# Optimization experiments

Hardware: AMD Instinct MI355X
Metric: run time of the kernel (lower is better)

Reference implementation:

```python
import jax, jax.numpy as jnp
import numpy as np

NUM_THRESHOLDS = 200
N = 4_000_000
KEPS = 1e-07
EPS = 1e-06


def _make_thresholds(num_thresholds=NUM_THRESHOLDS):
    inner = [(i + 1) * 1.0 / (num_thresholds - 1) for i in range(num_thresholds - 2)]
    return jnp.asarray([0.0 - KEPS] + inner + [1.0 + KEPS], dtype=jnp.float32)


def setup_inputs() -> dict:
    key = jax.random.key(0)
    k1, k2 = jax.random.split(key)
    predictions = jax.random.uniform(k1, (N,), dtype=jnp.float32)  # in [0,1]
    labels = jax.random.randint(k2, (N,), 0, 2, dtype=jnp.int32)
    thresholds = _make_thresholds()
    return {"predictions": predictions, "labels": labels, "thresholds": thresholds}


def reference(predictions, labels, thresholds):
    # Confusion matrix at all thresholds: [T, N] broadcast compare, reduce over N.
    lab_pos = labels.astype(bool)  # [N]
    pred_pos = predictions[None, :] > thresholds[:, None]  # [T, N] bool
    lab_pos_b = jnp.broadcast_to(lab_pos[None, :], pred_pos.shape)
    tp = jnp.sum(jnp.logical_and(lab_pos_b, pred_pos), axis=1).astype(jnp.float32)
    fn = jnp.sum(jnp.logical_and(lab_pos_b, ~pred_pos), axis=1).astype(jnp.float32)
    fp = jnp.sum(jnp.logical_and(~lab_pos_b, pred_pos), axis=1).astype(jnp.float32)
    tn = jnp.sum(jnp.logical_and(~lab_pos_b, ~pred_pos), axis=1).astype(jnp.float32)
    # Trapezoidal AUC over (FPR, TPR)
    rec = (tp + EPS) / (tp + fn + EPS)          # y (TPR)
    fp_rate = fp / (fp + tn + EPS)              # x (FPR)
    x, y = fp_rate, rec
    auc = jnp.sum((x[:-1] - x[1:]) * (y[:-1] + y[1:]) * 0.5)
    return auc
```

## Files before the change

kernel.cpp:

```cpp
#include <hip/hip_runtime.h>

#define NTH    200
#define NBINS  201
#define NBLKH  1024
#define HTPB   256
#define HWAVES 4


__device__ __forceinline__ void bin4(const float4 p, const int4 l,
                                     const float* __restrict__ s_th,
                                     unsigned int* __restrict__ my) {
    float pv[4] = {p.x, p.y, p.z, p.w};
    int   lv[4] = {l.x, l.y, l.z, l.w};
#pragma unroll
    for (int j = 0; j < 4; ++j) {
        float pp = pv[j];
        int k0 = (int)(pp * 199.0f);
        k0 = k0 > 198 ? 198 : k0;
        float ta = s_th[k0];
        float tb = s_th[k0 + 1];
        int g = k0 + ((ta < pp) ? ((tb < pp) ? 2 : 1) : 0);
        unsigned int add = 1u | ((unsigned int)(lv[j] != 0) << 16);
        atomicAdd(&my[g], add);
    }
}

__global__ void __launch_bounds__(HTPB)
auroc_hist_kernel(const float* __restrict__ preds,
                  const int*   __restrict__ labels,
                  const float* __restrict__ thresholds,
                  unsigned int* __restrict__ part,
                  unsigned int* __restrict__ ticket,
                  int n) {
    __shared__ float        s_th[NTH];
    __shared__ unsigned int s_hist[HWAVES][NBINS];

    const int t    = threadIdx.x;
    const int wave = t >> 6;

    if (blockIdx.x == 0 && t == 0) *ticket = 0u;

    for (int i = t; i < HWAVES * NBINS; i += HTPB)
        ((unsigned int*)s_hist)[i] = 0u;
    for (int i = t; i < NTH; i += HTPB)
        s_th[i] = thresholds[i];
    __syncthreads();

    unsigned int* my = s_hist[wave];

    const int gid = blockIdx.x * HTPB + t;
    const int S   = gridDim.x * HTPB;
    const int n4  = n >> 2;
    const float4* p4 = (const float4*)preds;
    const int4*   l4 = (const int4*)labels;

    int i = gid;
    for (; i + 3 * S < n4; i += 4 * S) {
        float4 pa = p4[i];
        float4 pb = p4[i + S];
        float4 pc = p4[i + 2 * S];
        float4 pd = p4[i + 3 * S];
        int4   la = l4[i];
        int4   lb = l4[i + S];
        int4   lc = l4[i + 2 * S];
        int4   ld = l4[i + 3 * S];
        bin4(pa, la, s_th, my);
        bin4(pb, lb, s_th, my);
        bin4(pc, lc, s_th, my);
        bin4(pd, ld, s_th, my);
    }
    for (; i < n4; i += S) {
        bin4(p4[i], l4[i], s_th, my);
    }
    for (int k = (n4 << 2) + gid; k < n; k += S) {
        float pp = preds[k];
        int k0 = (int)(pp * 199.0f);
        k0 = k0 > 198 ? 198 : k0;
        float ta = s_th[k0];
        float tb = s_th[k0 + 1];
        int g = k0 + ((ta < pp) ? ((tb < pp) ? 2 : 1) : 0);
        unsigned int add = 1u | ((unsigned int)(labels[k] != 0) << 16);
        atomicAdd(&my[g], add);
    }
    __syncthreads();

    const int b = blockIdx.x;
    for (int i2 = t; i2 < NBINS; i2 += HTPB) {
        unsigned int v = s_hist[0][i2] + s_hist[1][i2] + s_hist[2][i2] + s_hist[3][i2];
        unsigned int pos = v >> 16;
        unsigned int neg = (v & 0xFFFFu) - pos;
        part[i2 * NBLKH + b] = (pos << 16) | neg;
    }
}

__global__ void __launch_bounds__(256)
auroc_reduce_finish(const unsigned int* __restrict__ part,
                    unsigned int* __restrict__ g_pos,
                    unsigned int* __restrict__ g_neg,
                    unsigned int* __restrict__ ticket,
                    float* __restrict__ out) {
    __shared__ unsigned int s_w[HWAVES][2];
    __shared__ unsigned int s_rank;
    __shared__ unsigned int s_pos[NBINS], s_neg[NBINS];
    __shared__ unsigned int s_sufp[NBINS + 1], s_sufn[NBINS + 1];
    __shared__ float s_x[NTH], s_y[NTH];

    const int t = threadIdx.x;
    const int r = blockIdx.x;

    uint4 v = ((const uint4*)(part + r * NBLKH))[t];
    unsigned int ap = (v.x >> 16) + (v.y >> 16) + (v.z >> 16) + (v.w >> 16);
    unsigned int an = (v.x & 0xFFFFu) + (v.y & 0xFFFFu) +
                      (v.z & 0xFFFFu) + (v.w & 0xFFFFu);
#pragma unroll
    for (int off = 32; off >= 1; off >>= 1) {
        ap += __shfl_down(ap, off, 64);
        an += __shfl_down(an, off, 64);
    }
    if ((t & 63) == 0) { s_w[t >> 6][0] = ap; s_w[t >> 6][1] = an; }
    __syncthreads();

    if (t == 0) {
        unsigned int pos = s_w[0][0] + s_w[1][0] + s_w[2][0] + s_w[3][0];
        unsigned int neg = s_w[0][1] + s_w[1][1] + s_w[2][1] + s_w[3][1];
        atomicExch(&g_pos[r], pos);
        atomicExch(&g_neg[r], neg);
        __threadfence();
        s_rank = atomicAdd(ticket, 1u);
    }
    __syncthreads();
    if (s_rank != (unsigned int)(NBINS - 1)) return;

    __threadfence();
    if (t < NBINS) {
        s_pos[t] = atomicAdd(&g_pos[t], 0u);
        s_neg[t] = atomicAdd(&g_neg[t], 0u);
    }
    if (t == 0) { s_sufp[NBINS] = 0u; s_sufn[NBINS] = 0u; }
    __syncthreads();

    if (t < NBINS) {
        unsigned int sp = 0u, sn = 0u;
        for (int k = t; k < NBINS; ++k) { sp += s_pos[k]; sn += s_neg[k]; }
        s_sufp[t] = sp;
        s_sufn[t] = sn;
    }
    __syncthreads();

    const float P   = (float)s_sufp[0];
    const float Nn  = (float)s_sufn[0];
    const float EPS = 1e-6f;

    if (t < NTH) {
        float tp = (float)s_sufp[t + 1];
        float fp = (float)s_sufn[t + 1];
        float fn = P - tp;
        float tn = Nn - fp;
        s_y[t] = (tp + EPS) / (tp + fn + EPS);
        s_x[t] = fp / (fp + tn + EPS);
    }
    __syncthreads();

    if (t == 0) {
        double auc = 0.0;
        for (int i = 0; i < NTH - 1; ++i)
            auc += (double)((s_x[i] - s_x[i + 1]) * (s_y[i] + s_y[i + 1]) * 0.5f);
        out[0] = (float)auc;
    }
}

extern "C" void kernel_launch(void* const* d_in, const int* in_sizes, int n_in,
                              void* d_out, int out_size, void* d_ws, size_t ws_size,
                              hipStream_t stream) {
    const float* preds      = (const float*)d_in[0];
    const int*   labels     = (const int*)d_in[1];
    const float* thresholds = (const float*)d_in[2];
    float*       out        = (float*)d_out;
    unsigned int* part      = (unsigned int*)d_ws;
    unsigned int* g_pos     = part + NBINS * NBLKH;
    unsigned int* g_neg     = g_pos + NBINS;
    unsigned int* ticket    = g_neg + NBINS;

    const int n = in_sizes[0];

    auroc_hist_kernel<<<NBLKH, HTPB, 0, stream>>>(preds, labels, thresholds,
                                                  part, ticket, n);
    auroc_reduce_finish<<<NBINS, 256, 0, stream>>>(part, g_pos, g_neg,
                                                   ticket, out);
}
```

Baseline: 93.79 us.

## Split reduce into separate finish kernel; unroll hist by 2; branchless bin index

Replaces the last-block ticket/atomic handoff in the reduce kernel with a third single-block finish kernel, removing atomics and threadfences. The histogram main loop now processes two float4/int4 pairs per iteration instead of four, and the bin index uses summed comparisons instead of nested selects. The label is shifted directly without a !=0 test, which assumes labels are exactly 0 or 1. Adds one extra kernel launch and reduces memory-level parallelism per thread in the hist loop.

New measurement: 87.04 us. 1.08x faster.

```diff
diff --git a/kernel.cpp b/kernel.cpp
--- a/kernel.cpp
+++ b/kernel.cpp
@@ -6,31 +6,11 @@
 #define HTPB   256
 #define HWAVES 4
 
-
-__device__ __forceinline__ void bin4(const float4 p, const int4 l,
-                                     const float* __restrict__ s_th,
-                                     unsigned int* __restrict__ my) {
-    float pv[4] = {p.x, p.y, p.z, p.w};
-    int   lv[4] = {l.x, l.y, l.z, l.w};
-#pragma unroll
-    for (int j = 0; j < 4; ++j) {
-        float pp = pv[j];
-        int k0 = (int)(pp * 199.0f);
-        k0 = k0 > 198 ? 198 : k0;
-        float ta = s_th[k0];
-        float tb = s_th[k0 + 1];
-        int g = k0 + ((ta < pp) ? ((tb < pp) ? 2 : 1) : 0);
-        unsigned int add = 1u | ((unsigned int)(lv[j] != 0) << 16);
-        atomicAdd(&my[g], add);
-    }
-}
-
 __global__ void __launch_bounds__(HTPB)
 auroc_hist_kernel(const float* __restrict__ preds,
                   const int*   __restrict__ labels,
                   const float* __restrict__ thresholds,
                   unsigned int* __restrict__ part,
-                  unsigned int* __restrict__ ticket,
                   int n) {
     __shared__ float        s_th[NTH];
     __shared__ unsigned int s_hist[HWAVES][NBINS];
@@ -38,12 +18,10 @@
     const int t    = threadIdx.x;
     const int wave = t >> 6;
 
-    if (blockIdx.x == 0 && t == 0) *ticket = 0u;
-
+    for (int i = t; i < NTH; i += HTPB)
+        s_th[i] = thresholds[i];
     for (int i = t; i < HWAVES * NBINS; i += HTPB)
         ((unsigned int*)s_hist)[i] = 0u;
-    for (int i = t; i < NTH; i += HTPB)
-        s_th[i] = thresholds[i];
     __syncthreads();
 
     unsigned int* my = s_hist[wave];
@@ -55,22 +33,42 @@
     const int4*   l4 = (const int4*)labels;
 
     int i = gid;
-    for (; i + 3 * S < n4; i += 4 * S) {
+    for (; i + S < n4; i += 2 * S) {
         float4 pa = p4[i];
+        int4   la = l4[i];
         float4 pb = p4[i + S];
-        float4 pc = p4[i + 2 * S];
-        float4 pd = p4[i + 3 * S];
-        int4   la = l4[i];
         int4   lb = l4[i + S];
-        int4   lc = l4[i + 2 * S];
-        int4   ld = l4[i + 3 * S];
-        bin4(pa, la, s_th, my);
-        bin4(pb, lb, s_th, my);
-        bin4(pc, lc, s_th, my);
-        bin4(pd, ld, s_th, my);
+
+        float pv[8] = {pa.x, pa.y, pa.z, pa.w, pb.x, pb.y, pb.z, pb.w};
+        int   lv[8] = {la.x, la.y, la.z, la.w, lb.x, lb.y, lb.z, lb.w};
+#pragma unroll
+        for (int j = 0; j < 8; ++j) {
+            float pp = pv[j];
+            int k0 = (int)(pp * 199.0f);
+            k0 = k0 > 198 ? 198 : k0;
+            float ta = s_th[k0];
+            float tb = s_th[k0 + 1];
+            int g = k0 + (ta < pp) + (tb < pp);
+            unsigned int add = 1u | ((unsigned int)lv[j] << 16);
+            atomicAdd(&my[g], add);
+        }
     }
     for (; i < n4; i += S) {
-        bin4(p4[i], l4[i], s_th, my);
+        float4 p = p4[i];
+        int4   l = l4[i];
+        float pv[4] = {p.x, p.y, p.z, p.w};
+        int   lv[4] = {l.x, l.y, l.z, l.w};
+#pragma unroll
+        for (int j = 0; j < 4; ++j) {
+            float pp = pv[j];
+            int k0 = (int)(pp * 199.0f);
+            k0 = k0 > 198 ? 198 : k0;
+            float ta = s_th[k0];
+            float tb = s_th[k0 + 1];
+            int g = k0 + (ta < pp) + (tb < pp);
+            unsigned int add = 1u | ((unsigned int)lv[j] << 16);
+            atomicAdd(&my[g], add);
+        }
     }
     for (int k = (n4 << 2) + gid; k < n; k += S) {
         float pp = preds[k];
@@ -78,8 +76,8 @@
         k0 = k0 > 198 ? 198 : k0;
         float ta = s_th[k0];
         float tb = s_th[k0 + 1];
-        int g = k0 + ((ta < pp) ? ((tb < pp) ? 2 : 1) : 0);
-        unsigned int add = 1u | ((unsigned int)(labels[k] != 0) << 16);
+        int g = k0 + (ta < pp) + (tb < pp);
+        unsigned int add = 1u | ((unsigned int)labels[k] << 16);
         atomicAdd(&my[g], add);
     }
     __syncthreads();
@@ -94,16 +92,10 @@
 }
 
 __global__ void __launch_bounds__(256)
-auroc_reduce_finish(const unsigned int* __restrict__ part,
+auroc_reduce_kernel(const unsigned int* __restrict__ part,
                     unsigned int* __restrict__ g_pos,
-                    unsigned int* __restrict__ g_neg,
-                    unsigned int* __restrict__ ticket,
-                    float* __restrict__ out) {
+                    unsigned int* __restrict__ g_neg) {
     __shared__ unsigned int s_w[HWAVES][2];
-    __shared__ unsigned int s_rank;
-    __shared__ unsigned int s_pos[NBINS], s_neg[NBINS];
-    __shared__ unsigned int s_sufp[NBINS + 1], s_sufn[NBINS + 1];
-    __shared__ float s_x[NTH], s_y[NTH];
 
     const int t = threadIdx.x;
     const int r = blockIdx.x;
@@ -121,22 +113,23 @@
     __syncthreads();
 
     if (t == 0) {
-        unsigned int pos = s_w[0][0] + s_w[1][0] + s_w[2][0] + s_w[3][0];
-        unsigned int neg = s_w[0][1] + s_w[1][1] + s_w[2][1] + s_w[3][1];
-        atomicExch(&g_pos[r], pos);
-        atomicExch(&g_neg[r], neg);
-        __threadfence();
-        s_rank = atomicAdd(ticket, 1u);
+        g_pos[r] = s_w[0][0] + s_w[1][0] + s_w[2][0] + s_w[3][0];
+        g_neg[r] = s_w[0][1] + s_w[1][1] + s_w[2][1] + s_w[3][1];
     }
-    __syncthreads();
-    if (s_rank != (unsigned int)(NBINS - 1)) return;
+}
 
-    __threadfence();
-    if (t < NBINS) {
-        s_pos[t] = atomicAdd(&g_pos[t], 0u);
-        s_neg[t] = atomicAdd(&g_neg[t], 0u);
-    }
-    if (t == 0) { s_sufp[NBINS] = 0u; s_sufn[NBINS] = 0u; }
+__global__ void __launch_bounds__(256)
+auroc_finish_kernel(const unsigned int* __restrict__ g_pos,
+                    const unsigned int* __restrict__ g_neg,
+                    float* __restrict__ out) {
+    __shared__ unsigned int s_pos[NBINS], s_neg[NBINS];
+    __shared__ unsigned int s_sufp[NBINS + 1], s_sufn[NBINS + 1];
+    __shared__ float s_x[NTH], s_y[NTH];
+
+    const int t = threadIdx.x;
+
+    if (t < NBINS) { s_pos[t] = g_pos[t]; s_neg[t] = g_neg[t]; }
+    if (t == 0)    { s_sufp[NBINS] = 0u; s_sufn[NBINS] = 0u; }
     __syncthreads();
 
     if (t < NBINS) {
@@ -179,12 +172,11 @@
     unsigned int* part      = (unsigned int*)d_ws;
     unsigned int* g_pos     = part + NBINS * NBLKH;
     unsigned int* g_neg     = g_pos + NBINS;
-    unsigned int* ticket    = g_neg + NBINS;
 
     const int n = in_sizes[0];
 
     auroc_hist_kernel<<<NBLKH, HTPB, 0, stream>>>(preds, labels, thresholds,
-                                                  part, ticket, n);
-    auroc_reduce_finish<<<NBINS, 256, 0, stream>>>(part, g_pos, g_neg,
-                                                   ticket, out);
+                                                  part, n);
+    auroc_reduce_kernel<<<NBINS, 256, 0, stream>>>(part, g_pos, g_neg);
+    auroc_finish_kernel<<<1, 256, 0, stream>>>(g_pos, g_neg, out);
 }
```
